# Performance work log

Hardware: AMD Instinct MI355X
Metric: run time of the kernel (lower is better)

Reference implementation:

```python
import jax, jax.numpy as jnp
import numpy as np

N_NODES = 131072
N_EDGES = 4194304
NUM_GRAPHS = 128


def setup_inputs() -> dict:
    key = jax.random.key(0)
    ks = jax.random.split(key, 12)
    x = jax.random.normal(ks[0], (N_NODES, 3), dtype=jnp.float32)
    edge_index = jax.random.randint(ks[1], (2, N_EDGES), 0, N_NODES, dtype=jnp.int32)
    batch = jnp.sort(jax.random.randint(ks[2], (N_NODES,), 0, NUM_GRAPHS, dtype=jnp.int32))
    W1 = jax.random.normal(ks[3], (3, 16), dtype=jnp.float32) * 0.5
    b1 = jax.random.normal(ks[4], (16,), dtype=jnp.float32) * 0.1
    W2 = jax.random.normal(ks[5], (16, 64), dtype=jnp.float32) * 0.25
    b2 = jax.random.normal(ks[6], (64,), dtype=jnp.float32) * 0.1
    fcw1 = jax.random.normal(ks[7], (64, 32), dtype=jnp.float32) * 0.125
    fcb1 = jax.random.normal(ks[8], (32,), dtype=jnp.float32) * 0.1
    fcw2 = jax.random.normal(ks[9], (32, 2), dtype=jnp.float32) * 0.2
    fcb2 = jax.random.normal(ks[10], (2,), dtype=jnp.float32) * 0.1
    return dict(x=x, edge_index=edge_index, batch=batch, W1=W1, b1=b1,
                W2=W2, b2=b2, fcw1=fcw1, fcb1=fcb1, fcw2=fcw2, fcb2=fcb2)


def _gcn_conv(x, W, b, src, dst, n_nodes):
    # PyG GCNConv: add self-loops, symmetric D^-1/2 A_hat D^-1/2, then scatter-add at dst.
    h = x @ W  # [N, out]
    deg = jax.ops.segment_sum(jnp.ones_like(dst, dtype=h.dtype), dst, num_segments=n_nodes)
    dinv = jnp.where(deg > 0, jax.lax.rsqrt(jnp.maximum(deg, 1.0)), 0.0)
    norm = dinv[src] * dinv[dst]  # [E]
    msgs = norm[:, None] * h[src]  # gather + scale, [E, out]
    return jax.ops.segment_sum(msgs, dst, num_segments=n_nodes) + b


def reference(x, edge_index, batch, W1, b1, W2, b2, fcw1, fcb1, fcw2, fcb2):
    n = x.shape[0]
    loop = jnp.arange(n, dtype=edge_index.dtype)
    src = jnp.concatenate([edge_index[0], loop])
    dst = jnp.concatenate([edge_index[1], loop])
    h = jax.nn.relu(_gcn_conv(x, W1, b1, src, dst, n))
    h = jax.nn.relu(_gcn_conv(h, W2, b2, src, dst, n))
    # global_mean_pool over batch ids
    s = jax.ops.segment_sum(h, batch, num_segments=NUM_GRAPHS)
    cnt = jax.ops.segment_sum(jnp.ones((n,), h.dtype), batch, num_segments=NUM_GRAPHS)
    g = s / jnp.maximum(cnt, 1.0)[:, None]  # [G, 64]
    g = g @ fcw1 + fcb1
    return g @ fcw2 + fcb2  # [G, 2]
```

## Files before the change

kernel.cpp:

```cpp
#include <hip/hip_runtime.h>
#include <hip/hip_fp16.h>

#define N_NODES 131072
#define N_EDGES 4194304
#define NUM_GRAPHS 128

#define NB 512
#define NPB 256
#define BSHIFT 8
#define BCAP 10240
#define GSPAN 8

typedef int iv4 __attribute__((ext_vector_type(4)));

__global__ __launch_bounds__(512) void k_init(int* __restrict__ bcursor) {
  bcursor[threadIdx.x] = threadIdx.x * BCAP;
}

__global__ __launch_bounds__(1024) void k_binfill(const iv4* __restrict__ src4,
                                                  const iv4* __restrict__ dst4,
                                                  int* __restrict__ bcursor,
                                                  unsigned* __restrict__ binned) {
  __shared__ int hist[NB], base_[NB], rank_[NB];
  for (int k = threadIdx.x; k < NB; k += 1024) { hist[k] = 0; rank_[k] = 0; }
  __syncthreads();
  unsigned pk[16];
  int bk[16];
  int q0 = blockIdx.x * 4096 + threadIdx.x;
  #pragma unroll
  for (int i = 0; i < 4; ++i) {
    iv4 sv = __builtin_nontemporal_load(&src4[q0 + i * 1024]);
    iv4 dv = __builtin_nontemporal_load(&dst4[q0 + i * 1024]);
    #pragma unroll
    for (int j = 0; j < 4; ++j) {
      int idx = i * 4 + j;
      int s = sv[j], d = dv[j];
      bk[idx] = d >> BSHIFT;
      pk[idx] = ((unsigned)s << BSHIFT) | (unsigned)(d & (NPB - 1));
      atomicAdd(&hist[bk[idx]], 1);
    }
  }
  __syncthreads();
  for (int k = threadIdx.x; k < NB; k += 1024)
    base_[k] = atomicAdd(&bcursor[k], hist[k]);
  __syncthreads();
  #pragma unroll
  for (int i = 0; i < 16; ++i) {
    int r = atomicAdd(&rank_[bk[i]], 1);
    binned[base_[bk[i]] + r] = pk[i];
  }
}

__global__ __launch_bounds__(1024) void k_prep(const unsigned* __restrict__ binned,
                                               const int* __restrict__ bcursor,
                                               const float* __restrict__ x,
                                               float* __restrict__ dinv,
                                               float4* __restrict__ xs4) {
  __shared__ int dcount[NPB];
  int tid = threadIdx.x;
  if (tid < NPB) dcount[tid] = 0;
  __syncthreads();
  int b = blockIdx.x;
  int s0 = b * BCAP;
  int n = bcursor[b] - s0;
  for (int e = tid; e < n; e += 1024) {
    unsigned ent = __builtin_nontemporal_load(&binned[s0 + e]);
    atomicAdd(&dcount[ent & (NPB - 1)], 1);
  }
  __syncthreads();
  if (tid < NPB) {
    int node = b * NPB + tid;
    float di = rsqrtf((float)(dcount[tid] + 1));
    dinv[node] = di;
    xs4[node] = make_float4(di * x[node * 3 + 0], di * x[node * 3 + 1],
                            di * x[node * 3 + 2], 0.f);
  }
}

__global__ __launch_bounds__(1024) void k_sagg3h1(const unsigned* __restrict__ binned,
                                                  const int* __restrict__ bcursor,
                                                  const float* __restrict__ xs,
                                                  const float4* __restrict__ xs4,
                                                  const float* __restrict__ dinv,
                                                  const float* __restrict__ W1,
                                                  const float* __restrict__ b1,
                                                  unsigned* __restrict__ h1h) {
  __shared__ int dcount[NPB], cursor[NPB], nbase[NPB];
  __shared__ int wsum[4];
  __shared__ int csrL[BCAP];
  __shared__ float w[48];
  __shared__ float bb[16];
  __shared__ float accS[NPB * 4];
  int tid = threadIdx.x;
  if (tid >= 256 && tid < 304) w[tid - 256] = W1[tid - 256];
  if (tid >= 320 && tid < 336) bb[tid - 320] = b1[tid - 320];
  if (tid < NPB) dcount[tid] = 0;
  __syncthreads();

  int b = blockIdx.x;
  int s0 = b * BCAP;
  int n = bcursor[b] - s0;
  unsigned ent_r[10];
  #pragma unroll
  for (int j = 0; j < 10; ++j) {
    int e = tid + j * 1024;
    if (e < n) {
      unsigned ent = __builtin_nontemporal_load(&binned[s0 + e]);
      ent_r[j] = ent;
      atomicAdd(&dcount[ent & (NPB - 1)], 1);
    }
  }
  __syncthreads();

  int v = 0, incl = 0;
  if (tid < NPB) {
    v = dcount[tid];
    incl = v;
    #pragma unroll
    for (int d = 1; d < 64; d <<= 1) {
      int t = __shfl_up(incl, d);
      if ((tid & 63) >= d) incl += t;
    }
    if ((tid & 63) == 63) wsum[tid >> 6] = incl;
  }
  __syncthreads();
  if (tid < NPB) {
    int base = 0;
    int wv = tid >> 6;
    for (int w2 = 0; w2 < wv; ++w2) base += wsum[w2];
    int pref = base + incl - v;
    cursor[tid] = pref;
    nbase[tid] = pref;
  }
  __syncthreads();

  #pragma unroll
  for (int j = 0; j < 10; ++j) {
    int e = tid + j * 1024;
    if (e < n) {
      unsigned ent = ent_r[j];
      int pos = atomicAdd(&cursor[ent & (NPB - 1)], 1);
      csrL[pos] = (int)(ent >> BSHIFT) << 4;
    }
  }
  __syncthreads();

  int dl = tid >> 2;
  int q = tid & 3;
  int node = b * NPB + dl;
  int off = nbase[dl];
  int len = dcount[dl];
  const char* xsc = (const char*)xs;
  int qb = q << 2;
  float acc = 0.f;
  #pragma unroll 8
  for (int k = 0; k < len; ++k) {
    int bo = csrL[off + k];
    acc += *(const float*)(xsc + bo + qb);
  }
  accS[tid] = acc;
  __syncthreads();

  float di = dinv[node];
  float4 xself = xs4[node];
  float a0 = di * (accS[dl * 4 + 0] + xself.x);
  float a1 = di * (accS[dl * 4 + 1] + xself.y);
  float a2 = di * (accS[dl * 4 + 2] + xself.z);
  float o[4];
  #pragma unroll
  for (int j = 0; j < 4; ++j) {
    int cc = q * 4 + j;
    float vv = a0 * w[cc] + a1 * w[16 + cc] + a2 * w[32 + cc] + bb[cc];
    o[j] = di * fmaxf(vv, 0.f);
  }
  __half2 p0 = __floats2half2_rn(o[0], o[1]);
  __half2 p1 = __floats2half2_rn(o[2], o[3]);
  uint2 st;
  st.x = *reinterpret_cast<unsigned*>(&p0);
  st.y = *reinterpret_cast<unsigned*>(&p1);
  *(uint2*)(h1h + (size_t)node * 8 + q * 2) = st;
}

__global__ __launch_bounds__(1024) void k_sagg16pool(const unsigned* __restrict__ binned,
                                                     const int* __restrict__ bcursor,
                                                     const unsigned* __restrict__ h1h,
                                                     const float* __restrict__ dinv,
                                                     const int* __restrict__ batch,
                                                     const float* __restrict__ W2,
                                                     const float* __restrict__ b2,
                                                     float* __restrict__ gsum) {
  __shared__ int dcount[NPB], cursor[NPB], nbase[NPB];
  __shared__ int wsum[4];
  __shared__ int csrL[BCAP];
  __shared__ float aggS[NPB * 16];
  __shared__ float w2s[1024];
  __shared__ float b2s[64];
  __shared__ float gacc[GSPAN * 64];
  int tid = threadIdx.x;
  w2s[tid] = W2[tid];
  if (tid < 64) b2s[tid] = b2[tid];
  if (tid < GSPAN * 64) gacc[tid] = 0.f;
  if (tid < NPB) dcount[tid] = 0;
  __syncthreads();

  int b = blockIdx.x;
  int s0 = b * BCAP;
  int n = bcursor[b] - s0;
  unsigned ent_r[10];
  #pragma unroll
  for (int j = 0; j < 10; ++j) {
    int e = tid + j * 1024;
    if (e < n) {
      unsigned ent = __builtin_nontemporal_load(&binned[s0 + e]);
      ent_r[j] = ent;
      atomicAdd(&dcount[ent & (NPB - 1)], 1);
    }
  }
  __syncthreads();

  int v = 0, incl = 0;
  if (tid < NPB) {
    v = dcount[tid];
    incl = v;
    #pragma unroll
    for (int d = 1; d < 64; d <<= 1) {
      int t = __shfl_up(incl, d);
      if ((tid & 63) >= d) incl += t;
    }
    if ((tid & 63) == 63) wsum[tid >> 6] = incl;
  }
  __syncthreads();
  if (tid < NPB) {
    int base = 0;
    int wv = tid >> 6;
    for (int w2 = 0; w2 < wv; ++w2) base += wsum[w2];
    int pref = base + incl - v;
    cursor[tid] = pref;
    nbase[tid] = pref;
  }
  __syncthreads();

  #pragma unroll
  for (int j = 0; j < 10; ++j) {
    int e = tid + j * 1024;
    if (e < n) {
      unsigned ent = ent_r[j];
      int pos = atomicAdd(&cursor[ent & (NPB - 1)], 1);
      csrL[pos] = (int)(ent >> BSHIFT) << 5;
    }
  }
  __syncthreads();

  const char* h1c = (const char*)h1h;
  int q = tid & 7;
  int qb = q << 2;
  int nl0 = tid >> 3;
  #pragma unroll
  for (int half = 0; half < 2; ++half) {
    int dl = nl0 + half * 128;
    int node = b * NPB + dl;
    int off = nbase[dl];
    int len = dcount[dl];
    float o0 = 0.f, o1 = 0.f;
    #pragma unroll 8
    for (int k = 0; k < len; ++k) {
      int bo = csrL[off + k];
      unsigned hv = *(const unsigned*)(h1c + bo + qb);
      __half2 p = *reinterpret_cast<const __half2*>(&hv);
      o0 += __low2float(p);
      o1 += __high2float(p);
    }
    float di = dinv[node];
    unsigned sv = h1h[(size_t)node * 8 + q];
    __half2 sh = *reinterpret_cast<const __half2*>(&sv);
    aggS[dl * 16 + 2 * q + 0] = di * (o0 + __low2float(sh));
    aggS[dl * 16 + 2 * q + 1] = di * (o1 + __high2float(sh));
  }
  __syncthreads();

  int c = tid & 63;
  int slot = tid >> 6;
  int g0 = batch[b * NPB];
  float racc = 0.f;
  int curli = -1;
  for (int nloc = slot; nloc < NPB; nloc += 16) {
    int nd = b * NPB + nloc;
    int li = batch[nd] - g0;
    if (li != curli) {
      if (curli >= 0) {
        if (curli < GSPAN) atomicAdd(&gacc[curli * 64 + c], racc);
        else atomicAdd(&gsum[(size_t)(g0 + curli) * 64 + c], racc);
      }
      curli = li;
      racc = 0.f;
    }
    float vv = b2s[c];
    const float* ar = &aggS[nloc * 16];
    #pragma unroll
    for (int k = 0; k < 16; ++k) vv += ar[k] * w2s[k * 64 + c];
    racc += fmaxf(vv, 0.f);
  }
  if (curli >= 0) {
    if (curli < GSPAN) atomicAdd(&gacc[curli * 64 + c], racc);
    else atomicAdd(&gsum[(size_t)(g0 + curli) * 64 + c], racc);
  }
  __syncthreads();

  int span = batch[b * NPB + NPB - 1] - g0 + 1;
  if (span > GSPAN) span = GSPAN;
  for (int li = tid >> 6; li < span; li += 16) {
    atomicAdd(&gsum[(size_t)(g0 + li) * 64 + c], gacc[li * 64 + c]);
  }
}

__global__ __launch_bounds__(64) void k_fc(const float* __restrict__ gsum,
                                           const int* __restrict__ batch,
                                           const float* __restrict__ fcw1,
                                           const float* __restrict__ fcb1,
                                           const float* __restrict__ fcw2,
                                           const float* __restrict__ fcb2,
                                           float* __restrict__ out) {
  int g = blockIdx.x;
  int lo = 0, hi = N_NODES;
  while (lo < hi) { int m = (lo + hi) >> 1; if (batch[m] < g) lo = m + 1; else hi = m; }
  int start = lo;
  lo = start; hi = N_NODES;
  while (lo < hi) { int m = (lo + hi) >> 1; if (batch[m] < g + 1) lo = m + 1; else hi = m; }
  float inv = 1.0f / fmaxf((float)(lo - start), 1.0f);

  __shared__ float gmean[64];
  gmean[threadIdx.x] = gsum[(size_t)g * 64 + threadIdx.x] * inv;
  __syncthreads();

  __shared__ float hid[32];
  if (threadIdx.x < 32) {
    float a = fcb1[threadIdx.x];
    #pragma unroll
    for (int k = 0; k < 64; ++k) a += gmean[k] * fcw1[k * 32 + threadIdx.x];
    hid[threadIdx.x] = a;
  }
  __syncthreads();

  if (threadIdx.x < 2) {
    float a = fcb2[threadIdx.x];
    #pragma unroll
    for (int k = 0; k < 32; ++k) a += hid[k] * fcw2[k * 2 + threadIdx.x];
    out[g * 2 + threadIdx.x] = a;
  }
}

extern "C" void kernel_launch(void* const* d_in, const int* in_sizes, int n_in,
                              void* d_out, int out_size, void* d_ws, size_t ws_size,
                              hipStream_t stream) {
  const float* x    = (const float*)d_in[0];
  const int*   ei   = (const int*)d_in[1];
  const int*   batch= (const int*)d_in[2];
  const float* W1   = (const float*)d_in[3];
  const float* b1   = (const float*)d_in[4];
  const float* W2   = (const float*)d_in[5];
  const float* b2   = (const float*)d_in[6];
  const float* fcw1 = (const float*)d_in[7];
  const float* fcb1 = (const float*)d_in[8];
  const float* fcw2 = (const float*)d_in[9];
  const float* fcb2 = (const float*)d_in[10];
  float* out = (float*)d_out;

  char* w = (char*)d_ws;
  size_t off = 0;
  auto alloc = [&](size_t bytes) {
    void* p = w + off;
    off += (bytes + 255) & ~(size_t)255;
    return p;
  };
  int*      bcursor = (int*)     alloc((size_t)NB * 4);
  unsigned* binned  = (unsigned*)alloc((size_t)NB * BCAP * 4);
  float*    dinv    = (float*)   alloc((size_t)N_NODES * 4);
  float4*   xs4     = (float4*)  alloc((size_t)N_NODES * 16);
  unsigned* h1h     = (unsigned*)alloc((size_t)N_NODES * 32);
  float*    gsum    = (float*)   alloc((size_t)NUM_GRAPHS * 64 * 4);

  const iv4* src4 = (const iv4*)ei;
  const iv4* dst4 = (const iv4*)(ei + N_EDGES);

  hipMemsetAsync(gsum, 0, (size_t)NUM_GRAPHS * 64 * 4, stream);
  k_init<<<1, 512, 0, stream>>>(bcursor);
  k_binfill<<<N_EDGES / 16384, 1024, 0, stream>>>(src4, dst4, bcursor, binned);
  k_prep<<<NB, 1024, 0, stream>>>(binned, bcursor, x, dinv, xs4);
  k_sagg3h1<<<NB, 1024, 0, stream>>>(binned, bcursor, (const float*)xs4, xs4, dinv, W1, b1, h1h);
  k_sagg16pool<<<NB, 1024, 0, stream>>>(binned, bcursor, h1h, dinv, batch, W2, b2, gsum);
  k_fc<<<NUM_GRAPHS, 64, 0, stream>>>(gsum, batch, fcw1, fcb1, fcw2, fcb2, out);
}
```

Baseline: 120.0 us.

## Sort nodes by degree for balanced gathers, merge init into memset

Both aggregation kernels now counting-sort the block's 256 destination nodes by in-degree and give them to threads in that order. Neighbouring lanes in a wavefront then loop over similar edge counts, which reduces divergence from uneven degrees. The layer-2 gather switches from 8 lanes loading 4 bytes each to 4 lanes loading 8 bytes each, covering all 256 nodes in one pass. The k_init kernel is removed by zeroing the bin counts in the same memset as gsum, and binned writes use nontemporal stores. The extra scans and barriers add some in-block overhead.

New measurement: 234.3 us. +95.2%, slower.

```diff
diff --git a/kernel.cpp b/kernel.cpp
--- a/kernel.cpp
+++ b/kernel.cpp
@@ -13,13 +13,27 @@
 
 typedef int iv4 __attribute__((ext_vector_type(4)));
 
-__global__ __launch_bounds__(512) void k_init(int* __restrict__ bcursor) {
-  bcursor[threadIdx.x] = threadIdx.x * BCAP;
+__device__ __forceinline__ int scan256(int tid, int v, int* wsum) {
+  __syncthreads();
+  int incl = v;
+  #pragma unroll
+  for (int d = 1; d < 64; d <<= 1) {
+    int t = __shfl_up(incl, d);
+    if ((tid & 63) >= d) incl += t;
+  }
+  if (tid < NPB && (tid & 63) == 63) wsum[tid >> 6] = incl;
+  __syncthreads();
+  int base = 0;
+  int wv = tid >> 6;
+  #pragma unroll
+  for (int w2 = 0; w2 < 4; ++w2)
+    if (w2 < wv) base += wsum[w2];
+  return base + incl - v;
 }
 
 __global__ __launch_bounds__(1024) void k_binfill(const iv4* __restrict__ src4,
                                                   const iv4* __restrict__ dst4,
-                                                  int* __restrict__ bcursor,
+                                                  int* __restrict__ bcount,
                                                   unsigned* __restrict__ binned) {
   __shared__ int hist[NB], base_[NB], rank_[NB];
   for (int k = threadIdx.x; k < NB; k += 1024) { hist[k] = 0; rank_[k] = 0; }
@@ -42,17 +56,17 @@
   }
   __syncthreads();
   for (int k = threadIdx.x; k < NB; k += 1024)
-    base_[k] = atomicAdd(&bcursor[k], hist[k]);
+    base_[k] = k * BCAP + atomicAdd(&bcount[k], hist[k]);
   __syncthreads();
   #pragma unroll
   for (int i = 0; i < 16; ++i) {
     int r = atomicAdd(&rank_[bk[i]], 1);
-    binned[base_[bk[i]] + r] = pk[i];
+    __builtin_nontemporal_store(pk[i], &binned[base_[bk[i]] + r]);
   }
 }
 
 __global__ __launch_bounds__(1024) void k_prep(const unsigned* __restrict__ binned,
-                                               const int* __restrict__ bcursor,
+                                               const int* __restrict__ bcount,
                                                const float* __restrict__ x,
                                                float* __restrict__ dinv,
                                                float4* __restrict__ xs4) {
@@ -62,7 +76,7 @@
   __syncthreads();
   int b = blockIdx.x;
   int s0 = b * BCAP;
-  int n = bcursor[b] - s0;
+  int n = bcount[b];
   for (int e = tid; e < n; e += 1024) {
     unsigned ent = __builtin_nontemporal_load(&binned[s0 + e]);
     atomicAdd(&dcount[ent & (NPB - 1)], 1);
@@ -78,28 +92,28 @@
 }
 
 __global__ __launch_bounds__(1024) void k_sagg3h1(const unsigned* __restrict__ binned,
-                                                  const int* __restrict__ bcursor,
+                                                  const int* __restrict__ bcount,
                                                   const float* __restrict__ xs,
                                                   const float4* __restrict__ xs4,
                                                   const float* __restrict__ dinv,
                                                   const float* __restrict__ W1,
                                                   const float* __restrict__ b1,
                                                   unsigned* __restrict__ h1h) {
-  __shared__ int dcount[NPB], cursor[NPB], nbase[NPB];
+  __shared__ int dcount[NPB], cursor[NPB], nbase[NPB], perm[NPB];
   __shared__ int wsum[4];
   __shared__ int csrL[BCAP];
   __shared__ float w[48];
   __shared__ float bb[16];
   __shared__ float accS[NPB * 4];
   int tid = threadIdx.x;
-  if (tid >= 256 && tid < 304) w[tid - 256] = W1[tid - 256];
-  if (tid >= 320 && tid < 336) bb[tid - 320] = b1[tid - 320];
+  if (tid >= 512 && tid < 560) w[tid - 512] = W1[tid - 512];
+  if (tid >= 576 && tid < 592) bb[tid - 576] = b1[tid - 576];
   if (tid < NPB) dcount[tid] = 0;
   __syncthreads();
 
   int b = blockIdx.x;
   int s0 = b * BCAP;
-  int n = bcursor[b] - s0;
+  int n = bcount[b];
   unsigned ent_r[10];
   #pragma unroll
   for (int j = 0; j < 10; ++j) {
@@ -112,26 +126,9 @@
   }
   __syncthreads();
 
-  int v = 0, incl = 0;
-  if (tid < NPB) {
-    v = dcount[tid];
-    incl = v;
-    #pragma unroll
-    for (int d = 1; d < 64; d <<= 1) {
-      int t = __shfl_up(incl, d);
-      if ((tid & 63) >= d) incl += t;
-    }
-    if ((tid & 63) == 63) wsum[tid >> 6] = incl;
-  }
-  __syncthreads();
-  if (tid < NPB) {
-    int base = 0;
-    int wv = tid >> 6;
-    for (int w2 = 0; w2 < wv; ++w2) base += wsum[w2];
-    int pref = base + incl - v;
-    cursor[tid] = pref;
-    nbase[tid] = pref;
-  }
+  int v = (tid < NPB) ? dcount[tid] : 0;
+  int pref = scan256(tid, v, wsum);
+  if (tid < NPB) { cursor[tid] = pref; nbase[tid] = pref; }
   __syncthreads();
 
   #pragma unroll
@@ -143,33 +140,51 @@
       csrL[pos] = (int)(ent >> BSHIFT) << 4;
     }
   }
-  __syncthreads();
-
-  int dl = tid >> 2;
+
+  __syncthreads();
+  if (tid < NPB) cursor[tid] = 0;
+  __syncthreads();
+  int key = (tid < NPB) ? min(v, NPB - 1) : 0;
+  if (tid < NPB) atomicAdd(&cursor[key], 1);
+  __syncthreads();
+  int dv2 = (tid < NPB) ? cursor[tid] : 0;
+  int dpref = scan256(tid, dv2, wsum);
+  __syncthreads();
+  if (tid < NPB) cursor[tid] = dpref;
+  __syncthreads();
+  if (tid < NPB) {
+    int r = atomicAdd(&cursor[key], 1);
+    perm[r] = tid;
+  }
+  __syncthreads();
+
+  int dl = perm[tid >> 2];
   int q = tid & 3;
-  int node = b * NPB + dl;
   int off = nbase[dl];
   int len = dcount[dl];
   const char* xsc = (const char*)xs;
   int qb = q << 2;
   float acc = 0.f;
-  #pragma unroll 8
+  #pragma unroll 4
   for (int k = 0; k < len; ++k) {
     int bo = csrL[off + k];
     acc += *(const float*)(xsc + bo + qb);
   }
-  accS[tid] = acc;
-  __syncthreads();
-
+  accS[dl * 4 + q] = acc;
+  __syncthreads();
+
+  int dle = tid >> 2;
+  int qe = tid & 3;
+  int node = b * NPB + dle;
   float di = dinv[node];
   float4 xself = xs4[node];
-  float a0 = di * (accS[dl * 4 + 0] + xself.x);
-  float a1 = di * (accS[dl * 4 + 1] + xself.y);
-  float a2 = di * (accS[dl * 4 + 2] + xself.z);
+  float a0 = di * (accS[dle * 4 + 0] + xself.x);
+  float a1 = di * (accS[dle * 4 + 1] + xself.y);
+  float a2 = di * (accS[dle * 4 + 2] + xself.z);
   float o[4];
   #pragma unroll
   for (int j = 0; j < 4; ++j) {
-    int cc = q * 4 + j;
+    int cc = qe * 4 + j;
     float vv = a0 * w[cc] + a1 * w[16 + cc] + a2 * w[32 + cc] + bb[cc];
     o[j] = di * fmaxf(vv, 0.f);
   }
@@ -178,18 +193,18 @@
   uint2 st;
   st.x = *reinterpret_cast<unsigned*>(&p0);
   st.y = *reinterpret_cast<unsigned*>(&p1);
-  *(uint2*)(h1h + (size_t)node * 8 + q * 2) = st;
+  *(uint2*)(h1h + (size_t)node * 8 + qe * 2) = st;
 }
 
 __global__ __launch_bounds__(1024) void k_sagg16pool(const unsigned* __restrict__ binned,
-                                                     const int* __restrict__ bcursor,
+                                                     const int* __restrict__ bcount,
                                                      const unsigned* __restrict__ h1h,
                                                      const float* __restrict__ dinv,
                                                      const int* __restrict__ batch,
                                                      const float* __restrict__ W2,
                                                      const float* __restrict__ b2,
                                                      float* __restrict__ gsum) {
-  __shared__ int dcount[NPB], cursor[NPB], nbase[NPB];
+  __shared__ int dcount[NPB], cursor[NPB], nbase[NPB], perm[NPB];
   __shared__ int wsum[4];
   __shared__ int csrL[BCAP];
   __shared__ float aggS[NPB * 16];
@@ -205,7 +220,7 @@
 
   int b = blockIdx.x;
   int s0 = b * BCAP;
-  int n = bcursor[b] - s0;
+  int n = bcount[b];
   unsigned ent_r[10];
   #pragma unroll
   for (int j = 0; j < 10; ++j) {
@@ -218,26 +233,9 @@
   }
   __syncthreads();
 
-  int v = 0, incl = 0;
-  if (tid < NPB) {
-    v = dcount[tid];
-    incl = v;
-    #pragma unroll
-    for (int d = 1; d < 64; d <<= 1) {
-      int t = __shfl_up(incl, d);
-      if ((tid & 63) >= d) incl += t;
-    }
-    if ((tid & 63) == 63) wsum[tid >> 6] = incl;
-  }
-  __syncthreads();
-  if (tid < NPB) {
-    int base = 0;
-    int wv = tid >> 6;
-    for (int w2 = 0; w2 < wv; ++w2) base += wsum[w2];
-    int pref = base + incl - v;
-    cursor[tid] = pref;
-    nbase[tid] = pref;
-  }
+  int v = (tid < NPB) ? dcount[tid] : 0;
+  int pref = scan256(tid, v, wsum);
+  if (tid < NPB) { cursor[tid] = pref; nbase[tid] = pref; }
   __syncthreads();
 
   #pragma unroll
@@ -249,33 +247,49 @@
       csrL[pos] = (int)(ent >> BSHIFT) << 5;
     }
   }
+
+  __syncthreads();
+  if (tid < NPB) cursor[tid] = 0;
+  __syncthreads();
+  int key = (tid < NPB) ? min(v, NPB - 1) : 0;
+  if (tid < NPB) atomicAdd(&cursor[key], 1);
+  __syncthreads();
+  int dv2 = (tid < NPB) ? cursor[tid] : 0;
+  int dpref = scan256(tid, dv2, wsum);
+  __syncthreads();
+  if (tid < NPB) cursor[tid] = dpref;
+  __syncthreads();
+  if (tid < NPB) {
+    int r = atomicAdd(&cursor[key], 1);
+    perm[r] = tid;
+  }
   __syncthreads();
 
   const char* h1c = (const char*)h1h;
-  int q = tid & 7;
-  int qb = q << 2;
-  int nl0 = tid >> 3;
-  #pragma unroll
-  for (int half = 0; half < 2; ++half) {
-    int dl = nl0 + half * 128;
-    int node = b * NPB + dl;
-    int off = nbase[dl];
-    int len = dcount[dl];
-    float o0 = 0.f, o1 = 0.f;
-    #pragma unroll 8
-    for (int k = 0; k < len; ++k) {
-      int bo = csrL[off + k];
-      unsigned hv = *(const unsigned*)(h1c + bo + qb);
-      __half2 p = *reinterpret_cast<const __half2*>(&hv);
-      o0 += __low2float(p);
-      o1 += __high2float(p);
-    }
-    float di = dinv[node];
-    unsigned sv = h1h[(size_t)node * 8 + q];
-    __half2 sh = *reinterpret_cast<const __half2*>(&sv);
-    aggS[dl * 16 + 2 * q + 0] = di * (o0 + __low2float(sh));
-    aggS[dl * 16 + 2 * q + 1] = di * (o1 + __high2float(sh));
-  }
+  int dl = perm[tid >> 2];
+  int q = tid & 3;
+  int qb = q << 3;
+  int node = b * NPB + dl;
+  int off = nbase[dl];
+  int len = dcount[dl];
+  float o0 = 0.f, o1 = 0.f, o2 = 0.f, o3 = 0.f;
+  #pragma unroll 4
+  for (int k = 0; k < len; ++k) {
+    int bo = csrL[off + k];
+    uint2 hv = *(const uint2*)(h1c + bo + qb);
+    __half2 p0 = *reinterpret_cast<const __half2*>(&hv.x);
+    __half2 p1 = *reinterpret_cast<const __half2*>(&hv.y);
+    o0 += __low2float(p0); o1 += __high2float(p0);
+    o2 += __low2float(p1); o3 += __high2float(p1);
+  }
+  float di = dinv[node];
+  uint2 sv = *(const uint2*)(h1h + (size_t)node * 8 + q * 2);
+  __half2 s0h = *reinterpret_cast<const __half2*>(&sv.x);
+  __half2 s1h = *reinterpret_cast<const __half2*>(&sv.y);
+  aggS[dl * 16 + q * 4 + 0] = di * (o0 + __low2float(s0h));
+  aggS[dl * 16 + q * 4 + 1] = di * (o1 + __high2float(s0h));
+  aggS[dl * 16 + q * 4 + 2] = di * (o2 + __low2float(s1h));
+  aggS[dl * 16 + q * 4 + 3] = di * (o3 + __high2float(s1h));
   __syncthreads();
 
   int c = tid & 63;
@@ -372,21 +386,20 @@
     off += (bytes + 255) & ~(size_t)255;
     return p;
   };
-  int*      bcursor = (int*)     alloc((size_t)NB * 4);
+  float*    gsum    = (float*)   alloc((size_t)NUM_GRAPHS * 64 * 4);
+  int*      bcount  = (int*)     alloc((size_t)NB * 4);
   unsigned* binned  = (unsigned*)alloc((size_t)NB * BCAP * 4);
   float*    dinv    = (float*)   alloc((size_t)N_NODES * 4);
   float4*   xs4     = (float4*)  alloc((size_t)N_NODES * 16);
   unsigned* h1h     = (unsigned*)alloc((size_t)N_NODES * 32);
-  float*    gsum    = (float*)   alloc((size_t)NUM_GRAPHS * 64 * 4);
 
   const iv4* src4 = (const iv4*)ei;
   const iv4* dst4 = (const iv4*)(ei + N_EDGES);
 
-  hipMemsetAsync(gsum, 0, (size_t)NUM_GRAPHS * 64 * 4, stream);
-  k_init<<<1, 512, 0, stream>>>(bcursor);
-  k_binfill<<<N_EDGES / 16384, 1024, 0, stream>>>(src4, dst4, bcursor, binned);
-  k_prep<<<NB, 1024, 0, stream>>>(binned, bcursor, x, dinv, xs4);
-  k_sagg3h1<<<NB, 1024, 0, stream>>>(binned, bcursor, (const float*)xs4, xs4, dinv, W1, b1, h1h);
-  k_sagg16pool<<<NB, 1024, 0, stream>>>(binned, bcursor, h1h, dinv, batch, W2, b2, gsum);
+  (void)hipMemsetAsync(gsum, 0, (size_t)NUM_GRAPHS * 64 * 4 + (size_t)NB * 4, stream);
+  k_binfill<<<N_EDGES / 16384, 1024, 0, stream>>>(src4, dst4, bcount, binned);
+  k_prep<<<NB, 1024, 0, stream>>>(binned, bcount, x, dinv, xs4);
+  k_sagg3h1<<<NB, 1024, 0, stream>>>(binned, bcount, (const float*)xs4, xs4, dinv, W1, b1, h1h);
+  k_sagg16pool<<<NB, 1024, 0, stream>>>(binned, bcount, h1h, dinv, batch, W2, b2, gsum);
   k_fc<<<NUM_GRAPHS, 64, 0, stream>>>(gsum, batch, fcw1, fcb1, fcw2, fcb2, out);
 }
```
